# Performance work log

Measured on AMD Instinct MI355X. Metric: run time of the kernel, lower is better.

Reference implementation:

```python
import jax, jax.numpy as jnp
import numpy as np

B, N, D = 4, 8192, 512
L, W, S = 64, 64, 32  # num_tokens, win_size, stride


def setup_inputs() -> dict:
    key = jax.random.key(0)
    ks = jax.random.split(key, 12)
    inp = {
        "feats": jax.random.normal(ks[0], (B, N, D), jnp.float32),
        "coords": jax.random.normal(ks[1], (B, N, 2), jnp.float32) * 100.0,
        "mask": jnp.zeros((B, N), dtype=bool),
        "z": jax.random.normal(ks[2], (L, D), jnp.float32) * 0.02,
        "Wq": jax.random.normal(ks[3], (D, D), jnp.float32) * 0.01,
        "Wk": jax.random.normal(ks[4], (D, D), jnp.float32) * 0.01,
        "Wv": jax.random.normal(ks[5], (D, D), jnp.float32) * 0.01,
        "W1": jax.random.normal(ks[6], (D, 2), jnp.float32) * 0.05,
        "b1": jnp.zeros((D,), jnp.float32),
        "W2": jax.random.normal(ks[7], (D, D), jnp.float32) * 0.01,
        "b2": jnp.zeros((D,), jnp.float32),
        "Wo": jax.random.normal(ks[8], (D, D), jnp.float32) * 0.01,
        "bo": jnp.zeros((D,), jnp.float32),
    }
    return inp


def reference(feats, coords, mask, z, Wq, Wk, Wv, W1, b1, W2, b2, Wo, bo):
    # mask is all-False: every token valid, N_valid == N, segments are
    # contiguous blocks of P = N // L tokens (seg_id = floor(i*L/N)).
    Bz, Nn, Dd = feats.shape
    Ll = z.shape[0]
    P = Nn // Ll  # tokens per segment

    # LayerNorm over feature dim (no affine, eps=1e-5 as in F.layer_norm)
    mu = feats.mean(-1, keepdims=True)
    var = feats.var(-1, keepdims=True)
    f_ln = (feats - mu) * jax.lax.rsqrt(var + 1e-5)

    # per-sample coordinate normalization (torch std is unbiased, ddof=1)
    c_mu = coords.mean(1, keepdims=True)
    c_sd = coords.std(1, keepdims=True, ddof=1) + 1e-8
    c_n = (coords - c_mu) / c_sd

    f_seg = f_ln.reshape(Bz, Ll, P, Dd)
    c_seg = c_n.reshape(Bz, Ll, P, 2)

    # static sliding windows within each segment (last window may be partial)
    starts = np.arange(0, P, S)                      # [nw]
    idx = starts[:, None] + np.arange(W)[None, :]    # [nw, W]
    valid = jnp.asarray(idx < P)                     # [nw, W] bool
    idx_c = np.minimum(idx, P - 1)
    cnt = valid.sum(-1).astype(feats.dtype)          # [nw]

    f_win = f_seg[:, :, idx_c]                       # [B,L,nw,W,D]
    c_win = c_seg[:, :, idx_c]                       # [B,L,nw,W,2]

    vmask = valid.astype(feats.dtype)[None, None, :, :, None]
    c_mean = (c_win * vmask).sum(3) / cnt[None, None, :, None]   # [B,L,nw,2]
    pos_in = c_win - c_mean[:, :, :, None, :]
    h = jax.nn.relu(jnp.einsum('blnwc,dc->blnwd', pos_in, W1) + b1)
    pos_bias = jnp.einsum('blnwd,ed->blnwe', h, W2) + b2

    q = z @ Wq.T                                     # [L,D]
    k = jnp.einsum('blnwd,ed->blnwe', f_win, Wk) + pos_bias
    v = jnp.einsum('blnwd,ed->blnwe', f_win, Wv)

    temperature = jnp.sqrt(jnp.asarray(Dd, feats.dtype))
    logits = jnp.einsum('ld,blnwd->blnw', q, k) / temperature
    logits = jnp.clip(logits, -10.0, 10.0)
    logits = jnp.where(valid[None, None], logits, -jnp.inf)
    attn = jax.nn.softmax(logits, axis=-1)           # [B,L,nw,W]

    z_win = jnp.einsum('blnw,blnwd->blnd', attn, v)  # [B,L,nw,D]
    z_l = z_win.mean(2)                              # average over windows
    return z_l @ Wo.T + bo                           # [B,L,D]
```

## Files before the change

kernel.cpp:

```cpp
#include <hip/hip_runtime.h>

#define Bz 4
#define Nn 8192
#define Dd 512
#define Ll 64
#define Pp 128
#define Ww 64
#define Ss 32
#define NW 4

#define WPI(d) ((d) + 2 * ((d) >> 7))

__global__ __launch_bounds__(256) void pre1(
    const float* __restrict__ coords, const float* __restrict__ b2,
    const float* __restrict__ Wq, const float* __restrict__ Wk,
    const float* __restrict__ W2,
    const float* __restrict__ Wv, const float* __restrict__ Wo,
    float* __restrict__ cstats,
    float* __restrict__ M1, float* __restrict__ M2,
    float* __restrict__ WvoT, float* __restrict__ vb8) {
    __shared__ float As[64][68];
    __shared__ float Bs[64][68];
    __shared__ float b2s[64];
    __shared__ double dred[16];
    int bid = blockIdx.x, tid = threadIdx.x;
    int wv = tid >> 6, lane = tid & 63;

    if (bid < 192) {
        int role = bid >> 6;
        int wb = bid & 63;
        int m0 = (wb >> 3) * 64;
        int n0 = (wb & 7) * 64;
        const float* Amat = (role == 2) ? Wv : Wq;
        const float* Bmat = (role == 0) ? Wk : (role == 1) ? W2 : Wo;
        float* Cmat = (role == 0) ? M1 : (role == 1) ? M2 : WvoT;
        int tx = tid & 15, ty = tid >> 4;
        float4 acc[4];
#pragma unroll
        for (int i = 0; i < 4; ++i) acc[i] = make_float4(0.f, 0.f, 0.f, 0.f);

        for (int k0 = 0; k0 < Dd; k0 += 64) {
            {
                int kk = tid >> 4, q4 = (tid & 15) * 4;
#pragma unroll
                for (int i = 0; i < 4; ++i) {
                    int k = kk + 16 * i;
                    *(float4*)&As[k][q4] =
                        *(const float4*)&Amat[(size_t)(k0 + k) * Dd + m0 + q4];
                }
                if (role != 2) {
#pragma unroll
                    for (int i = 0; i < 4; ++i) {
                        int k = kk + 16 * i;
                        *(float4*)&Bs[k][q4] =
                            *(const float4*)&Bmat[(size_t)(k0 + k) * Dd + n0 + q4];
                    }
                } else {
                    int d = tid >> 2;
#pragma unroll
                    for (int j = 0; j < 4; ++j) {
                        int c0 = (tid & 3) * 16 + 4 * j;
                        float4 v = *(const float4*)&Bmat[(size_t)(n0 + d) * Dd + k0 + c0];
                        Bs[c0 + 0][d] = v.x; Bs[c0 + 1][d] = v.y;
                        Bs[c0 + 2][d] = v.z; Bs[c0 + 3][d] = v.w;
                    }
                }
            }
            __syncthreads();
#pragma unroll 8
            for (int kk = 0; kk < 64; ++kk) {
                float4 a4 = *(const float4*)&As[kk][ty * 4];
                float4 b4 = *(const float4*)&Bs[kk][tx * 4];
                acc[0].x = fmaf(a4.x, b4.x, acc[0].x); acc[0].y = fmaf(a4.x, b4.y, acc[0].y);
                acc[0].z = fmaf(a4.x, b4.z, acc[0].z); acc[0].w = fmaf(a4.x, b4.w, acc[0].w);
                acc[1].x = fmaf(a4.y, b4.x, acc[1].x); acc[1].y = fmaf(a4.y, b4.y, acc[1].y);
                acc[1].z = fmaf(a4.y, b4.z, acc[1].z); acc[1].w = fmaf(a4.y, b4.w, acc[1].w);
                acc[2].x = fmaf(a4.z, b4.x, acc[2].x); acc[2].y = fmaf(a4.z, b4.y, acc[2].y);
                acc[2].z = fmaf(a4.z, b4.z, acc[2].z); acc[2].w = fmaf(a4.z, b4.w, acc[2].w);
                acc[3].x = fmaf(a4.w, b4.x, acc[3].x); acc[3].y = fmaf(a4.w, b4.y, acc[3].y);
                acc[3].z = fmaf(a4.w, b4.z, acc[3].z); acc[3].w = fmaf(a4.w, b4.w, acc[3].w);
            }
            __syncthreads();
        }
#pragma unroll
        for (int i = 0; i < 4; ++i)
            *(float4*)&Cmat[(size_t)(m0 + ty * 4 + i) * Dd + n0 + tx * 4] = acc[i];
    } else if (bid < 200) {
        int j = bid - 192;
        if (tid < 64) b2s[tid] = b2[j * 64 + tid];
        __syncthreads();
        float a0 = 0.f, a1 = 0.f;
#pragma unroll 4
        for (int ee = 0; ee < 64; ++ee) {
            int e = j * 64 + ee;
            float be = b2s[ee];
            a0 = fmaf(be, Wq[(size_t)e * Dd + tid], a0);
            a1 = fmaf(be, Wq[(size_t)e * Dd + tid + 256], a1);
        }
        vb8[j * Dd + tid] = a0;
        vb8[j * Dd + tid + 256] = a1;
    } else {
        int b = bid - 200;
        double sx = 0, sy = 0, sxx = 0, syy = 0;
        const float4* cp = (const float4*)(coords + (size_t)b * Nn * 2);
        for (int i = tid; i < Nn / 2; i += 256) {
            float4 v = cp[i];
            sx  += (double)v.x + (double)v.z;
            sy  += (double)v.y + (double)v.w;
            sxx += (double)v.x * v.x + (double)v.z * v.z;
            syy += (double)v.y * v.y + (double)v.w * v.w;
        }
        for (int o = 32; o > 0; o >>= 1) {
            sx  += __shfl_down(sx,  o); sy  += __shfl_down(sy,  o);
            sxx += __shfl_down(sxx, o); syy += __shfl_down(syy, o);
        }
        if (lane == 0) {
            dred[wv * 4 + 0] = sx;  dred[wv * 4 + 1] = sy;
            dred[wv * 4 + 2] = sxx; dred[wv * 4 + 3] = syy;
        }
        __syncthreads();
        if (tid == 0) {
            double tx = 0, ty = 0, txx = 0, tyy = 0;
            for (int i = 0; i < 4; ++i) {
                tx += dred[i * 4 + 0]; ty += dred[i * 4 + 1];
                txx += dred[i * 4 + 2]; tyy += dred[i * 4 + 3];
            }
            const double N = (double)Nn;
            double mux = tx / N, muy = ty / N;
            double vx = (txx - N * mux * mux) / (N - 1.0);
            double vy = (tyy - N * muy * muy) / (N - 1.0);
            cstats[b * 4 + 0] = (float)mux;
            cstats[b * 4 + 1] = (float)muy;
            cstats[b * 4 + 2] = (float)sqrt(vx) + 1e-8f;
            cstats[b * 4 + 3] = (float)sqrt(vy) + 1e-8f;
        }
    }
}

__global__ __launch_bounds__(256) void qkg_k(
    const float* __restrict__ z, const float* __restrict__ M1,
    const float* __restrict__ M2, const float* __restrict__ vb8,
    float* __restrict__ QK, float* __restrict__ G,
    float* __restrict__ sqk4, float* __restrict__ qb2) {
    __shared__ float zs[Dd];
    __shared__ float pq[8][128];
    __shared__ float pg[8][128];
    __shared__ float red[8];
    int bid = blockIdx.x, tid = threadIdx.x;
    int l = bid & 63, ch = bid >> 6;
    int wv = tid >> 6, lane = tid & 63;

    zs[tid]       = z[(size_t)l * Dd + tid];
    zs[tid + 256] = z[(size_t)l * Dd + tid + 256];
    __syncthreads();

    if (ch == 0) {
        float vba = 0.f, vbb = 0.f;
#pragma unroll
        for (int j = 0; j < 8; ++j) {
            vba += vb8[j * Dd + tid];
            vbb += vb8[j * Dd + tid + 256];
        }
        float p = zs[tid] * vba + zs[tid + 256] * vbb;
        for (int o = 32; o > 0; o >>= 1) p += __shfl_xor(p, o);
        if (lane == 0) red[4 + wv] = p;
    }

    {
        int qd = tid & 31, h = tid >> 5;
        int cb = ch * 128 + qd * 4;
        float4 aq = make_float4(0.f, 0.f, 0.f, 0.f);
        float4 ag = make_float4(0.f, 0.f, 0.f, 0.f);
        for (int d = h * 64; d < h * 64 + 64; ++d) {
            float zd = zs[d];
            float4 m1 = *(const float4*)&M1[(size_t)d * Dd + cb];
            float4 m2 = *(const float4*)&M2[(size_t)d * Dd + cb];
            aq.x = fmaf(zd, m1.x, aq.x); aq.y = fmaf(zd, m1.y, aq.y);
            aq.z = fmaf(zd, m1.z, aq.z); aq.w = fmaf(zd, m1.w, aq.w);
            ag.x = fmaf(zd, m2.x, ag.x); ag.y = fmaf(zd, m2.y, ag.y);
            ag.z = fmaf(zd, m2.z, ag.z); ag.w = fmaf(zd, m2.w, ag.w);
        }
        *(float4*)&pq[h][qd * 4] = aq;
        *(float4*)&pg[h][qd * 4] = ag;
    }
    __syncthreads();
    if (tid < 128) {
        float vq = 0.f, vg = 0.f;
#pragma unroll
        for (int hh = 0; hh < 8; ++hh) { vq += pq[hh][tid]; vg += pg[hh][tid]; }
        QK[(size_t)l * Dd + ch * 128 + tid] = vq;
        G [(size_t)l * Dd + ch * 128 + tid] = vg;
        float s = vq;
        for (int o = 32; o > 0; o >>= 1) s += __shfl_xor(s, o);
        if (lane == 0) red[wv] = s;
    }
    __syncthreads();
    if (tid == 0) sqk4[ch * 64 + l] = red[0] + red[1];
    if (ch == 0 && tid == 32) qb2[l] = red[4] + red[5] + red[6] + red[7];
}

__global__ __launch_bounds__(1024) void attn2(
    const float* __restrict__ feats, const float* __restrict__ coords,
    const float* __restrict__ cstats,
    const float* __restrict__ QKm, const float* __restrict__ Gm,
    const float* __restrict__ sqk4, const float* __restrict__ qb2,
    const float* __restrict__ W1, const float* __restrict__ b1,
    const float* __restrict__ WvoT, const float* __restrict__ bo,
    float* __restrict__ out) {
    __shared__ float  qk_s[Dd];
    __shared__ float4 wpack[Dd + 8];
    __shared__ float  scx[Pp], scy[Pp];
    __shared__ float  smu[Pp], srs[Pp], sa[Pp];
    __shared__ float  shs[NW * Ww];
    __shared__ float  sar[NW][Ww];
    __shared__ float  swt[Pp];
    __shared__ float  s2red[NW];
    __shared__ float  soff;
    __shared__ float  red16[16][Dd];

    int bx = blockIdx.x;
    int l = bx & 63, b = bx >> 6;
    int tid = threadIdx.x;
    int wv = tid >> 6, lane = tid & 63;

    if (tid < Dd) {
        qk_s[tid] = QKm[l * Dd + tid];
    } else {
        int t = tid - Dd;
        wpack[WPI(t)] = make_float4(W1[2 * t], W1[2 * t + 1], b1[t], Gm[l * Dd + t]);
    }
    if (tid < Pp) {
        int row = bx * Pp + tid;
        float x = coords[(size_t)row * 2], y = coords[(size_t)row * 2 + 1];
        scx[tid] = (x - cstats[b * 4 + 0]) / cstats[b * 4 + 2];
        scy[tid] = (y - cstats[b * 4 + 1]) / cstats[b * 4 + 3];
    }
    float sqk_l = sqk4[l] + sqk4[64 + l] + sqk4[128 + l] + sqk4[192 + l];
    float qb2_l = qb2[l];
    __syncthreads();

    const float* fbase = feats + (size_t)bx * Pp * Dd;
    int rb = wv * 8;
    float4 f0[8], f1[8];
#pragma unroll
    for (int i = 0; i < 8; ++i) {
        const float4* fr = (const float4*)(fbase + (size_t)(rb + i) * Dd);
        f0[i] = fr[lane];
        f1[i] = fr[lane + 64];
    }
    __builtin_amdgcn_sched_barrier(0);

    float cmx[4], cmy[4];
#pragma unroll
    for (int n = 0; n < 4; ++n) {
        int nv = (n == 3) ? 32 : 64;
        float cx = (lane < nv) ? scx[n * Ss + lane] : 0.f;
        float cy = (lane < nv) ? scy[n * Ss + lane] : 0.f;
        for (int o = 32; o > 0; o >>= 1) { cx += __shfl_xor(cx, o); cy += __shfl_xor(cy, o); }
        cmx[n] = cx / (float)nv; cmy[n] = cy / (float)nv;
    }

    {
        int s = tid >> 2, q = tid & 3;
        int n = s >> 6, w = s & 63;
        int nv = (n == 3) ? 32 : 64;
        float hs = 0.f;
        if (w < nv) {
            int p = n * Ss + w;
            float px = scx[p] - cmx[n], py = scy[p] - cmy[n];
            int d0 = q * 128;
#pragma unroll 4
            for (int i = 0; i < 128; ++i) {
                float4 c = wpack[WPI(d0) + i];
                hs = fmaf(c.w, fmaxf(fmaf(c.x, px, fmaf(c.y, py, c.z)), 0.f), hs);
            }
        }
        hs += __shfl_xor(hs, 1);
        hs += __shfl_xor(hs, 2);
        if (q == 0) shs[s] = hs;
    }

    {
        float4 q0 = ((const float4*)qk_s)[lane];
        float4 q1 = ((const float4*)qk_s)[lane + 64];
#pragma unroll
        for (int b2i = 0; b2i < 8; b2i += 4) {
            float sP[4], ssP[4], aP[4];
#pragma unroll
            for (int i = 0; i < 4; ++i) {
                float4 v0 = f0[b2i + i], v1 = f1[b2i + i];
                sP[i]  = v0.x + v0.y + v0.z + v0.w + v1.x + v1.y + v1.z + v1.w;
                ssP[i] = v0.x * v0.x + v0.y * v0.y + v0.z * v0.z + v0.w * v0.w
                       + v1.x * v1.x + v1.y * v1.y + v1.z * v1.z + v1.w * v1.w;
                aP[i]  = v0.x * q0.x + v0.y * q0.y + v0.z * q0.z + v0.w * q0.w
                       + v1.x * q1.x + v1.y * q1.y + v1.z * q1.z + v1.w * q1.w;
            }
#pragma unroll
            for (int o = 32; o > 0; o >>= 1) {
#pragma unroll
                for (int i = 0; i < 4; ++i) {
                    sP[i] += __shfl_xor(sP[i], o); ssP[i] += __shfl_xor(ssP[i], o);
                    aP[i] += __shfl_xor(aP[i], o);
                }
            }
            if (lane == 0) {
#pragma unroll
                for (int i = 0; i < 4; ++i) {
                    int r = rb + b2i + i;
                    float mu  = sP[i] * (1.f / (float)Dd);
                    float var = ssP[i] * (1.f / (float)Dd) - mu * mu;
                    smu[r] = mu; srs[r] = 1.f / sqrtf(var + 1e-5f); sa[r] = aP[i];
                }
            }
        }
    }
    __syncthreads();

    const float invtemp = 0.04419417382415922f;
    if (wv < 4) {
        int n = wv, w = lane;
        int nv = (n == 3) ? 32 : 64;
        int p = n * Ss + ((w < nv) ? w : 0);
        float lg = -1e30f;
        if (w < nv) {
            lg = (srs[p] * (sa[p] - smu[p] * sqk_l) + shs[n * Ww + w] + qb2_l) * invtemp;
            lg = fminf(fmaxf(lg, -10.f), 10.f);
        }
        float m = lg;
        for (int o = 32; o > 0; o >>= 1) m = fmaxf(m, __shfl_xor(m, o));
        float e = (w < nv) ? expf(lg - m) : 0.f;
        float ssum = e;
        for (int o = 32; o > 0; o >>= 1) ssum += __shfl_xor(ssum, o);
        float ar = (w < nv) ? (e / ssum) * srs[p] : 0.f;
        sar[n][w] = ar;
        float t2 = (w < nv) ? ar * smu[p] : 0.f;
        for (int o = 32; o > 0; o >>= 1) t2 += __shfl_xor(t2, o);
        if (lane == 0) s2red[n] = t2;
    }
    __syncthreads();

    if (tid < Pp) {
        int p = tid;
        int na = (p >> 5) - 1, nb = (p >> 5);
        float wt = 0.f;
        if (na >= 0 && na <= 3) wt += sar[na][p - na * Ss];
        if (nb <= 3)            wt += sar[nb][p - nb * Ss];
        swt[p] = wt;
    }
    if (tid == 0) soff = 0.25f * (s2red[0] + s2red[1] + s2red[2] + s2red[3]);
    __syncthreads();

    {
        float4 a0 = make_float4(0.f, 0.f, 0.f, 0.f);
        float4 a1 = make_float4(0.f, 0.f, 0.f, 0.f);
#pragma unroll
        for (int i = 0; i < 8; ++i) {
            float wt = swt[rb + i];
            a0.x = fmaf(wt, f0[i].x, a0.x); a0.y = fmaf(wt, f0[i].y, a0.y);
            a0.z = fmaf(wt, f0[i].z, a0.z); a0.w = fmaf(wt, f0[i].w, a0.w);
            a1.x = fmaf(wt, f1[i].x, a1.x); a1.y = fmaf(wt, f1[i].y, a1.y);
            a1.z = fmaf(wt, f1[i].z, a1.z); a1.w = fmaf(wt, f1[i].w, a1.w);
        }
        *(float4*)&red16[wv][lane * 4]       = a0;
        *(float4*)&red16[wv][256 + lane * 4] = a1;
    }
    __syncthreads();
    if (tid < Dd) {
        float v = 0.f;
#pragma unroll
        for (int w = 0; w < 16; ++w) v += red16[w][tid];
        qk_s[tid] = 0.25f * v - soff;
    }
    __syncthreads();

    {
        int h = tid >> 7, cq = (tid & 127) * 4;
        float4 acc = make_float4(0.f, 0.f, 0.f, 0.f);
#pragma unroll 4
        for (int e = h * 64; e < h * 64 + 64; ++e) {
            float fe = qk_s[e];
            float4 w = *(const float4*)&WvoT[(size_t)e * Dd + cq];
            acc.x = fmaf(fe, w.x, acc.x);
            acc.y = fmaf(fe, w.y, acc.y);
            acc.z = fmaf(fe, w.z, acc.z);
            acc.w = fmaf(fe, w.w, acc.w);
        }
        *(float4*)&red16[h][cq] = acc;
    }
    __syncthreads();
    if (tid < Dd) {
        out[(size_t)bx * Dd + tid] = bo[tid]
            + red16[0][tid] + red16[1][tid] + red16[2][tid] + red16[3][tid]
            + red16[4][tid] + red16[5][tid] + red16[6][tid] + red16[7][tid];
    }
}

extern "C" void kernel_launch(void* const* d_in, const int* in_sizes, int n_in,
                              void* d_out, int out_size, void* d_ws, size_t ws_size,
                              hipStream_t stream) {
    const float* feats  = (const float*)d_in[0];
    const float* coords = (const float*)d_in[1];
    const float* z  = (const float*)d_in[3];
    const float* Wq = (const float*)d_in[4];
    const float* Wk = (const float*)d_in[5];
    const float* Wv = (const float*)d_in[6];
    const float* W1 = (const float*)d_in[7];
    const float* b1 = (const float*)d_in[8];
    const float* W2 = (const float*)d_in[9];
    const float* b2 = (const float*)d_in[10];
    const float* Wo = (const float*)d_in[11];
    const float* bo = (const float*)d_in[12];
    float* out = (float*)d_out;

    float* ws = (float*)d_ws;
    float* cstats = ws;
    float* M1     = ws + 16;
    float* M2     = M1 + Dd * Dd;
    float* WvoT   = M2 + Dd * Dd;
    float* vb8    = WvoT + Dd * Dd;
    float* QK     = vb8 + 8 * Dd;
    float* G      = QK + Ll * Dd;
    float* sqk4   = G + Ll * Dd;
    float* qb2    = sqk4 + 256;

    pre1<<<204, 256, 0, stream>>>(coords, b2, Wq, Wk, W2, Wv, Wo,
                                  cstats, M1, M2, WvoT, vb8);
    qkg_k<<<256, 256, 0, stream>>>(z, M1, M2, vb8, QK, G, sqk4, qb2);
    attn2<<<Bz * Ll, 1024, 0, stream>>>(feats, coords, cstats,
                                        QK, G, sqk4, qb2, W1, b1,
                                        WvoT, bo, out);
}
```

Before: 167.2 us.

## Split each segment across two blocks by window pair and merge outputs with atomics

```diff
diff --git a/kernel.cpp b/kernel.cpp
--- a/kernel.cpp
+++ b/kernel.cpp
@@ -16,9 +16,11 @@
     const float* __restrict__ Wq, const float* __restrict__ Wk,
     const float* __restrict__ W2,
     const float* __restrict__ Wv, const float* __restrict__ Wo,
+    const float* __restrict__ bo,
     float* __restrict__ cstats,
     float* __restrict__ M1, float* __restrict__ M2,
-    float* __restrict__ WvoT, float* __restrict__ vb8) {
+    float* __restrict__ WvoT, float* __restrict__ vb8,
+    float* __restrict__ out) {
     __shared__ float As[64][68];
     __shared__ float Bs[64][68];
     __shared__ float b2s[64];
@@ -99,7 +101,7 @@
         }
         vb8[j * Dd + tid] = a0;
         vb8[j * Dd + tid + 256] = a1;
-    } else {
+    } else if (bid < 204) {
         int b = bid - 200;
         double sx = 0, sy = 0, sxx = 0, syy = 0;
         const float4* cp = (const float4*)(coords + (size_t)b * Nn * 2);
@@ -133,6 +135,12 @@
             cstats[b * 4 + 1] = (float)muy;
             cstats[b * 4 + 2] = (float)sqrt(vx) + 1e-8f;
             cstats[b * 4 + 3] = (float)sqrt(vy) + 1e-8f;
+        }
+    } else {
+        int j = bid - 204;
+        for (int i = tid; i < 16384; i += 256) {
+            int idx = j * 16384 + i;
+            out[idx] = bo[idx & (Dd - 1)];
         }
     }
 }
@@ -199,38 +207,40 @@
     if (ch == 0 && tid == 32) qb2[l] = red[4] + red[5] + red[6] + red[7];
 }
 
-__global__ __launch_bounds__(1024) void attn2(
+__global__ __launch_bounds__(768) void attn2h(
     const float* __restrict__ feats, const float* __restrict__ coords,
     const float* __restrict__ cstats,
     const float* __restrict__ QKm, const float* __restrict__ Gm,
     const float* __restrict__ sqk4, const float* __restrict__ qb2,
     const float* __restrict__ W1, const float* __restrict__ b1,
-    const float* __restrict__ WvoT, const float* __restrict__ bo,
+    const float* __restrict__ WvoT,
     float* __restrict__ out) {
     __shared__ float  qk_s[Dd];
     __shared__ float4 wpack[Dd + 8];
     __shared__ float  scx[Pp], scy[Pp];
     __shared__ float  smu[Pp], srs[Pp], sa[Pp];
-    __shared__ float  shs[NW * Ww];
-    __shared__ float  sar[NW][Ww];
+    __shared__ float  shs[2 * Ww];
+    __shared__ float  sar[2][Ww];
     __shared__ float  swt[Pp];
-    __shared__ float  s2red[NW];
-    __shared__ float  soff;
-    __shared__ float  red16[16][Dd];
-
-    int bx = blockIdx.x;
-    int l = bx & 63, b = bx >> 6;
+    __shared__ float  s2red[2];
+    __shared__ float  soffp;
+    __shared__ float  red12[12][Dd];
+
+    int g = blockIdx.x;
+    int seg = g >> 1, half = g & 1;
+    int l = seg & 63, b = seg >> 6;
     int tid = threadIdx.x;
     int wv = tid >> 6, lane = tid & 63;
+    int r0 = half ? 64 : 0;
+    int nrw = half ? 8 : 12;
 
     if (tid < Dd) {
         qk_s[tid] = QKm[l * Dd + tid];
-    } else {
-        int t = tid - Dd;
-        wpack[WPI(t)] = make_float4(W1[2 * t], W1[2 * t + 1], b1[t], Gm[l * Dd + t]);
+        wpack[WPI(tid)] = make_float4(W1[2 * tid], W1[2 * tid + 1], b1[tid],
+                                      Gm[l * Dd + tid]);
     }
     if (tid < Pp) {
-        int row = bx * Pp + tid;
+        int row = seg * Pp + tid;
         float x = coords[(size_t)row * 2], y = coords[(size_t)row * 2 + 1];
         scx[tid] = (x - cstats[b * 4 + 0]) / cstats[b * 4 + 2];
         scy[tid] = (y - cstats[b * 4 + 1]) / cstats[b * 4 + 3];
@@ -239,35 +249,34 @@
     float qb2_l = qb2[l];
     __syncthreads();
 
-    const float* fbase = feats + (size_t)bx * Pp * Dd;
-    int rb = wv * 8;
+    const float* fbase = feats + (size_t)seg * Pp * Dd;
+    int rb = r0 + wv * 8;
     float4 f0[8], f1[8];
-#pragma unroll
-    for (int i = 0; i < 8; ++i) {
-        const float4* fr = (const float4*)(fbase + (size_t)(rb + i) * Dd);
-        f0[i] = fr[lane];
-        f1[i] = fr[lane + 64];
+    if (wv < nrw) {
+#pragma unroll
+        for (int i = 0; i < 8; ++i) {
+            const float4* fr = (const float4*)(fbase + (size_t)(rb + i) * Dd);
+            f0[i] = fr[lane];
+            f1[i] = fr[lane + 64];
+        }
     }
     __builtin_amdgcn_sched_barrier(0);
 
-    float cmx[4], cmy[4];
-#pragma unroll
-    for (int n = 0; n < 4; ++n) {
+    if (tid < 512) {
+        int s = tid >> 2, q = tid & 3;
+        int nloc = s >> 6, w = s & 63;
+        int n = half * 2 + nloc;
         int nv = (n == 3) ? 32 : 64;
+
         float cx = (lane < nv) ? scx[n * Ss + lane] : 0.f;
         float cy = (lane < nv) ? scy[n * Ss + lane] : 0.f;
         for (int o = 32; o > 0; o >>= 1) { cx += __shfl_xor(cx, o); cy += __shfl_xor(cy, o); }
-        cmx[n] = cx / (float)nv; cmy[n] = cy / (float)nv;
-    }
-
-    {
-        int s = tid >> 2, q = tid & 3;
-        int n = s >> 6, w = s & 63;
-        int nv = (n == 3) ? 32 : 64;
+        float cmxn = cx / (float)nv, cmyn = cy / (float)nv;
+
         float hs = 0.f;
         if (w < nv) {
             int p = n * Ss + w;
-            float px = scx[p] - cmx[n], py = scy[p] - cmy[n];
+            float px = scx[p] - cmxn, py = scy[p] - cmyn;
             int d0 = q * 128;
 #pragma unroll 4
             for (int i = 0; i < 128; ++i) {
@@ -277,10 +286,10 @@
         }
         hs += __shfl_xor(hs, 1);
         hs += __shfl_xor(hs, 2);
-        if (q == 0) shs[s] = hs;
-    }
-
-    {
+        if (q == 0) shs[nloc * Ww + w] = hs;
+    }
+
+    if (wv < nrw) {
         float4 q0 = ((const float4*)qk_s)[lane];
         float4 q1 = ((const float4*)qk_s)[lane + 64];
 #pragma unroll
@@ -317,13 +326,14 @@
     __syncthreads();
 
     const float invtemp = 0.04419417382415922f;
-    if (wv < 4) {
-        int n = wv, w = lane;
+    if (wv < 2) {
+        int nloc = wv, w = lane;
+        int n = half * 2 + nloc;
         int nv = (n == 3) ? 32 : 64;
         int p = n * Ss + ((w < nv) ? w : 0);
         float lg = -1e30f;
         if (w < nv) {
-            lg = (srs[p] * (sa[p] - smu[p] * sqk_l) + shs[n * Ww + w] + qb2_l) * invtemp;
+            lg = (srs[p] * (sa[p] - smu[p] * sqk_l) + shs[nloc * Ww + w] + qb2_l) * invtemp;
             lg = fminf(fmaxf(lg, -10.f), 10.f);
         }
         float m = lg;
@@ -332,25 +342,29 @@
         float ssum = e;
         for (int o = 32; o > 0; o >>= 1) ssum += __shfl_xor(ssum, o);
         float ar = (w < nv) ? (e / ssum) * srs[p] : 0.f;
-        sar[n][w] = ar;
+        sar[nloc][w] = ar;
         float t2 = (w < nv) ? ar * smu[p] : 0.f;
         for (int o = 32; o > 0; o >>= 1) t2 += __shfl_xor(t2, o);
-        if (lane == 0) s2red[n] = t2;
+        if (lane == 0) s2red[nloc] = t2;
     }
     __syncthreads();
 
     if (tid < Pp) {
         int p = tid;
-        int na = (p >> 5) - 1, nb = (p >> 5);
         float wt = 0.f;
-        if (na >= 0 && na <= 3) wt += sar[na][p - na * Ss];
-        if (nb <= 3)            wt += sar[nb][p - nb * Ss];
+#pragma unroll
+        for (int nloc = 0; nloc < 2; ++nloc) {
+            int n = half * 2 + nloc;
+            int nv = (n == 3) ? 32 : 64;
+            int w = p - n * Ss;
+            if (w >= 0 && w < nv) wt += sar[nloc][w];
+        }
         swt[p] = wt;
     }
-    if (tid == 0) soff = 0.25f * (s2red[0] + s2red[1] + s2red[2] + s2red[3]);
-    __syncthreads();
-
-    {
+    if (tid == 0) soffp = 0.25f * (s2red[0] + s2red[1]);
+    __syncthreads();
+
+    if (wv < nrw) {
         float4 a0 = make_float4(0.f, 0.f, 0.f, 0.f);
         float4 a1 = make_float4(0.f, 0.f, 0.f, 0.f);
 #pragma unroll
@@ -361,23 +375,23 @@
             a1.x = fmaf(wt, f1[i].x, a1.x); a1.y = fmaf(wt, f1[i].y, a1.y);
             a1.z = fmaf(wt, f1[i].z, a1.z); a1.w = fmaf(wt, f1[i].w, a1.w);
         }
-        *(float4*)&red16[wv][lane * 4]       = a0;
-        *(float4*)&red16[wv][256 + lane * 4] = a1;
+        *(float4*)&red12[wv][lane * 4]       = a0;
+        *(float4*)&red12[wv][256 + lane * 4] = a1;
     }
     __syncthreads();
     if (tid < Dd) {
         float v = 0.f;
-#pragma unroll
-        for (int w = 0; w < 16; ++w) v += red16[w][tid];
-        qk_s[tid] = 0.25f * v - soff;
+        for (int w = 0; w < nrw; ++w) v += red12[w][tid];
+        qk_s[tid] = 0.25f * v - soffp;
     }
     __syncthreads();
 
     {
         int h = tid >> 7, cq = (tid & 127) * 4;
+        int e0 = h * 86, e1 = (e0 + 86 < Dd) ? e0 + 86 : Dd;
         float4 acc = make_float4(0.f, 0.f, 0.f, 0.f);
-#pragma unroll 4
-        for (int e = h * 64; e < h * 64 + 64; ++e) {
+#pragma unroll 2
+        for (int e = e0; e < e1; ++e) {
             float fe = qk_s[e];
             float4 w = *(const float4*)&WvoT[(size_t)e * Dd + cq];
             acc.x = fmaf(fe, w.x, acc.x);
@@ -385,13 +399,13 @@
             acc.z = fmaf(fe, w.z, acc.z);
             acc.w = fmaf(fe, w.w, acc.w);
         }
-        *(float4*)&red16[h][cq] = acc;
+        *(float4*)&red12[h][cq] = acc;
     }
     __syncthreads();
     if (tid < Dd) {
-        out[(size_t)bx * Dd + tid] = bo[tid]
-            + red16[0][tid] + red16[1][tid] + red16[2][tid] + red16[3][tid]
-            + red16[4][tid] + red16[5][tid] + red16[6][tid] + red16[7][tid];
+        float v = red12[0][tid] + red12[1][tid] + red12[2][tid]
+                + red12[3][tid] + red12[4][tid] + red12[5][tid];
+        atomicAdd(&out[(size_t)seg * Dd + tid], v);
     }
 }
 
@@ -423,10 +437,10 @@
     float* sqk4   = G + Ll * Dd;
     float* qb2    = sqk4 + 256;
 
-    pre1<<<204, 256, 0, stream>>>(coords, b2, Wq, Wk, W2, Wv, Wo,
-                                  cstats, M1, M2, WvoT, vb8);
+    pre1<<<212, 256, 0, stream>>>(coords, b2, Wq, Wk, W2, Wv, Wo, bo,
+                                  cstats, M1, M2, WvoT, vb8, out);
     qkg_k<<<256, 256, 0, stream>>>(z, M1, M2, vb8, QK, G, sqk4, qb2);
-    attn2<<<Bz * Ll, 1024, 0, stream>>>(feats, coords, cstats,
-                                        QK, G, sqk4, qb2, W1, b1,
-                                        WvoT, bo, out);
+    attn2h<<<2 * Bz * Ll, 768, 0, stream>>>(feats, coords, cstats,
+                                            QK, G, sqk4, qb2, W1, b1,
+                                            WvoT, out);
 }
```

Measured after the change: 188.6 us. 1.13x slower.
